# Optimization experiments

Hardware: AMD Instinct MI355X
Metric: run time of the kernel (lower is better)

## Reference

```python
import jax, jax.numpy as jnp
import numpy as np

GROUPS = 32
EPS = 1e-5

def setup_inputs() -> dict:
    key = jax.random.key(0)
    ks = jax.random.split(key, 10)
    B, H, W, C = 2, 64, 64, 512
    s = 1.0 / np.sqrt(C)
    return {
        "x": jax.random.normal(ks[0], (B, H, W, C), dtype=jnp.float32),
        "gamma": jnp.ones((C,), jnp.float32),
        "beta": jnp.zeros((C,), jnp.float32),
        "wq": jax.random.normal(ks[1], (C, C), jnp.float32) * s,
        "bq": jnp.zeros((C,), jnp.float32),
        "wk": jax.random.normal(ks[2], (C, C), jnp.float32) * s,
        "bk": jnp.zeros((C,), jnp.float32),
        "wv": jax.random.normal(ks[3], (C, C), jnp.float32) * s,
        "bv": jnp.zeros((C,), jnp.float32),
        "wp": jax.random.normal(ks[4], (C, C), jnp.float32) * s,
        "bp": jnp.zeros((C,), jnp.float32),
    }

def _group_norm(x, gamma, beta):
    B, H, W, C = x.shape
    xg = x.reshape(B, H, W, GROUPS, C // GROUPS)
    mean = jnp.mean(xg, axis=(1, 2, 4), keepdims=True)
    var = jnp.var(xg, axis=(1, 2, 4), keepdims=True)
    xg = (xg - mean) * jax.lax.rsqrt(var + EPS)
    return xg.reshape(B, H, W, C) * gamma + beta

def reference(x, gamma, beta, wq, bq, wk, bk, wv, bv, wp, bp):
    B, H, W, C = x.shape
    h_ = _group_norm(x, gamma, beta)
    # 1x1 convs are per-pixel linear maps
    q = jnp.einsum("bhwc,cd->bhwd", h_, wq) + bq
    k = jnp.einsum("bhwc,cd->bhwd", h_, wk) + bk
    v = jnp.einsum("bhwc,cd->bhwd", h_, wv) + bv
    q = q.reshape(B, H * W, C)
    k = k.reshape(B, H * W, C)
    v = v.reshape(B, H * W, C)
    scale = C ** (-0.5)
    attn = jax.nn.softmax(jnp.einsum("bqc,bkc->bqk", q, k) * scale, axis=-1)
    out = jnp.einsum("bqk,bkc->bqc", attn, v).reshape(B, H, W, C)
    proj = jnp.einsum("bhwc,cd->bhwd", out, wp) + bp
    return x + proj
```

## Files before the change

kernel.cpp:

```cpp
#include <hip/hip_runtime.h>
#include <hip/hip_bf16.h>
#include <cstdint>
#include <cstddef>

typedef __bf16 bf16;
typedef bf16 bf16x8 __attribute__((ext_vector_type(8)));
typedef bf16 bf16x4 __attribute__((ext_vector_type(4)));
typedef float floatx4 __attribute__((ext_vector_type(4)));
typedef int intx8 __attribute__((ext_vector_type(8)));
typedef int intx4 __attribute__((ext_vector_type(4)));

#define DEVI __device__ __forceinline__

#define C_  512
#define HW_ 4096
#define B_  2
#define M_  8192
#define TK  64


DEVI floatx4 mfma16(bf16x8 a, bf16x8 b, floatx4 c) {
  return __builtin_amdgcn_mfma_f32_16x16x32_bf16(a, b, c, 0, 0, 0);
}

DEVI floatx4 mfma_fp8(intx8 a, intx8 b, floatx4 c) {
  return __builtin_amdgcn_mfma_scale_f32_16x16x128_f8f6f4(a, b, c, 0, 0,
                                                          0, 127, 0, 127);
}

DEVI void gload16(const void* g, void* lds) {
  using gp = const __attribute__((address_space(1))) unsigned int*;
  using lp = __attribute__((address_space(3))) unsigned int*;
  __builtin_amdgcn_global_load_lds(
      reinterpret_cast<gp>(reinterpret_cast<uintptr_t>(g)),
      reinterpret_cast<lp>((unsigned int)(uintptr_t)lds), 16, 0, 0);
}

template <int N> DEVI void wait_vmcnt() {
  if constexpr (N == 0)       asm volatile("s_waitcnt vmcnt(0)" ::: "memory");
  else if constexpr (N == 6)  asm volatile("s_waitcnt vmcnt(6)" ::: "memory");
  else if constexpr (N == 8)  asm volatile("s_waitcnt vmcnt(8)" ::: "memory");
  else static_assert(N == 0, "unsupported vmcnt literal");
}

DEVI uint32_t f32_to_fp8(float x) {
  return (uint32_t)__builtin_amdgcn_cvt_pk_fp8_f32(x, x, 0, false) & 0xffu;
}
DEVI int pack4_fp8(float a, float b, float c, float d) {
  int pk = __builtin_amdgcn_cvt_pk_fp8_f32(a, b, 0, false);
  return __builtin_amdgcn_cvt_pk_fp8_f32(c, d, pk, true);
}

__global__ __launch_bounds__(256) void gn_part(const float* __restrict__ x,
                                               float* __restrict__ pp,
                                               float* __restrict__ l) {
  int blk = blockIdx.x;
  int t = threadIdx.x;
  if (t < 16) l[blk * 16 + t] = 0.f;
  int batch = blk >> 8;
  int pix0 = (blk & 255) * 16;
  int c4 = (t & 127) << 2;
  int ph = t >> 7;
  const float* px = x + (size_t)batch * HW_ * C_ + (size_t)(pix0 + ph) * C_ + c4;
  float s1 = 0.f, s2 = 0.f;
#pragma unroll
  for (int i = 0; i < 8; i++) {
    float4 v = *reinterpret_cast<const float4*>(px + (size_t)i * 2 * C_);
    s1 += v.x + v.y + v.z + v.w;
    s2 += v.x * v.x + v.y * v.y + v.z * v.z + v.w * v.w;
  }
  __shared__ float l1[256], l2[256];
  l1[t] = s1; l2[t] = s2;
  __syncthreads();
  if (t < 32) {
    float a = 0.f, b2 = 0.f;
#pragma unroll
    for (int j = 0; j < 4; j++) {
      a  += l1[t * 4 + j] + l1[t * 4 + j + 128];
      b2 += l2[t * 4 + j] + l2[t * 4 + j + 128];
    }
    pp[blk * 32 + t] = a;
    pp[512 * 32 + blk * 32 + t] = b2;
  }
}

__global__ __launch_bounds__(256) void finish_wtrans(
    const float* __restrict__ pp, float* __restrict__ stats,
    const float* __restrict__ wq, const float* __restrict__ wk,
    const float* __restrict__ wv, const float* __restrict__ wp,
    uint8_t* __restrict__ w8, bf16* __restrict__ wtp) {
  int t = threadIdx.x;
  if (blockIdx.x < 64) {
    int bg = blockIdx.x;
    int b = bg >> 5, g = bg & 31;
    float s1 = pp[(b * 256 + t) * 32 + g];
    float s2 = pp[512 * 32 + (b * 256 + t) * 32 + g];
    for (int off = 32; off; off >>= 1) {
      s1 += __shfl_down(s1, off);
      s2 += __shfl_down(s2, off);
    }
    __shared__ float r1[4], r2[4];
    int wid = t >> 6;
    if ((t & 63) == 0) { r1[wid] = s1; r2[wid] = s2; }
    __syncthreads();
    if (t == 0) {
      s1 = r1[0] + r1[1] + r1[2] + r1[3];
      s2 = r2[0] + r2[1] + r2[2] + r2[3];
      float inv = 1.0f / (HW_ * 16);
      float mean = s1 * inv;
      float var  = s2 * inv - mean * mean;
      stats[bg]      = mean;
      stats[64 + bg] = rsqrtf(var + 1e-5f);
    }
    return;
  }
  int id = blockIdx.x - 64;
  int z = id >> 8;
  int k0 = ((id >> 4) & 15) * 32, n0 = (id & 15) * 32;
  const float* w = (z == 0) ? wq : (z == 1) ? wk : (z == 2) ? wv : wp;
  __shared__ float tt[32][33];
  int r = t >> 5, cc = t & 31;
  for (int i = 0; i < 4; i++) {
    int rr = r + i * 8;
    tt[rr][cc] = w[(size_t)(k0 + rr) * C_ + n0 + cc];
  }
  __syncthreads();
  if (z < 3) {
    uint8_t* dst = w8 + (size_t)z * C_ * C_;
    for (int i = 0; i < 4; i++) {
      int rr = r + i * 8;
      dst[(size_t)(n0 + rr) * C_ + k0 + cc] = (uint8_t)f32_to_fp8(tt[cc][rr]);
    }
  } else {
    for (int i = 0; i < 4; i++) {
      int rr = r + i * 8;
      wtp[(size_t)(n0 + rr) * C_ + k0 + cc] = (bf16)tt[cc][rr];
    }
  }
}

__global__ __launch_bounds__(256) void gn_apply(const float* __restrict__ x,
                                                const float* __restrict__ gamma,
                                                const float* __restrict__ beta,
                                                const float* __restrict__ stats,
                                                uint8_t* __restrict__ h8) {
  int idx = blockIdx.x * 256 + threadIdx.x;
  int m  = idx >> 7;
  int c4 = (idx & 127) << 2;
  int b = m >> 12;
  int g = c4 >> 4;
  float mean = stats[(b << 5) + g];
  float rs   = stats[64 + (b << 5) + g];
  const float4 xv = *reinterpret_cast<const float4*>(x + (size_t)m * C_ + c4);
  const float4 gv = *reinterpret_cast<const float4*>(gamma + c4);
  const float4 bv = *reinterpret_cast<const float4*>(beta + c4);
  int pk = pack4_fp8((xv.x - mean) * rs * gv.x + bv.x,
                     (xv.y - mean) * rs * gv.y + bv.y,
                     (xv.z - mean) * rs * gv.z + bv.z,
                     (xv.w - mean) * rs * gv.w + bv.w);
  *reinterpret_cast<int*>(h8 + (size_t)m * C_ + c4) = pk;
}

template <int BM, int BN, int MT, int NT>
DEVI void gemm_main(const bf16* __restrict__ A, int lda,
                    const bf16* __restrict__ Bt, int ldb,
                    int K, floatx4 (&acc)[MT][NT]) {
  constexpr int WCOLS = BN / (NT * 16);
  constexpr int NLD = BM / 32 + BN / 32;
  static_assert(NLD == 6 || NLD == 8, "vmcnt literal supports 6/8");
  __shared__ __align__(16) bf16 As[2][BM * TK];
  __shared__ __align__(16) bf16 Bs[2][BN * TK];
  int tid = threadIdx.x;
  int w = tid >> 6, lane = tid & 63;
  int wrow = w / WCOLS, wcol = w % WCOLS;
  int col = lane & 15, quad = lane >> 4;
#pragma unroll
  for (int mt = 0; mt < MT; mt++)
#pragma unroll
    for (int nt = 0; nt < NT; nt++)
      acc[mt][nt] = floatx4{0.f, 0.f, 0.f, 0.f};

  auto stage = [&](int k0, bf16* as, bf16* bs) {
#pragma unroll
    for (int i = 0; i < BM / 32; i++) {
      int id = tid + i * 256;
      int r = id >> 3, wd = id & 7;
      gload16(A + (size_t)r * lda + k0 + ((wd ^ (r & 7)) << 3), as + id * 8);
    }
#pragma unroll
    for (int i = 0; i < BN / 32; i++) {
      int id = tid + i * 256;
      int r = id >> 3, wd = id & 7;
      gload16(Bt + (size_t)r * ldb + k0 + ((wd ^ (r & 7)) << 3), bs + id * 8);
    }
  };
  auto compute = [&](const bf16* sa, const bf16* sb) {
#pragma unroll
    for (int kk = 0; kk < 2; kk++) {
      bf16x8 af[MT], bfr[NT];
#pragma unroll
      for (int mt = 0; mt < MT; mt++) {
        int rA = wrow * MT * 16 + mt * 16 + col;
        af[mt] = *reinterpret_cast<const bf16x8*>(
            sa + rA * TK + (((kk * 4 + quad) ^ (rA & 7)) << 3));
      }
#pragma unroll
      for (int nt = 0; nt < NT; nt++) {
        int rB = wcol * NT * 16 + nt * 16 + col;
        bfr[nt] = *reinterpret_cast<const bf16x8*>(
            sb + rB * TK + (((kk * 4 + quad) ^ (rB & 7)) << 3));
      }
#pragma unroll
      for (int mt = 0; mt < MT; mt++)
#pragma unroll
        for (int nt = 0; nt < NT; nt++)
          acc[mt][nt] = mfma16(af[mt], bfr[nt], acc[mt][nt]);
    }
  };

  bf16 *s0a = &As[0][0], *s0b = &Bs[0][0];
  bf16 *s1a = &As[1][0], *s1b = &Bs[1][0];
  stage(0, s0a, s0b);
  int nIter = K / TK;
  for (int t = 0; t < nIter - 1; t++) {
    stage((t + 1) * TK, s1a, s1b);
    wait_vmcnt<NLD>();
    asm volatile("s_barrier" ::: "memory");
    compute(s0a, s0b);
    asm volatile("s_waitcnt lgkmcnt(0)" ::: "memory");
    asm volatile("s_barrier" ::: "memory");
    bf16* tp;
    tp = s0a; s0a = s1a; s1a = tp;
    tp = s0b; s0b = s1b; s1b = tp;
  }
  wait_vmcnt<0>();
  asm volatile("s_barrier" ::: "memory");
  compute(s0a, s0b);
}

template <int BM, int BN, int MT, int NT, int THREADS>
DEVI void gemm_fp8(const uint8_t* __restrict__ A, int lda,
                   const uint8_t* __restrict__ Bt, int ldb,
                   int K, floatx4 (&acc)[MT][NT]) {
  constexpr int WCOLS = BN / (NT * 16);
  constexpr int RPP = THREADS / 8;
  constexpr int NLD = (BM + BN) / RPP;
  static_assert(NLD == 6 || NLD == 8, "vmcnt literal supports 6/8");
  static_assert(BM % RPP == 0 && BN % RPP == 0, "stage pass mismatch");
  __shared__ __align__(16) uint8_t As[2][BM * 128];
  __shared__ __align__(16) uint8_t Bs[2][BN * 128];
  int tid = threadIdx.x;
  int w = tid >> 6, lane = tid & 63;
  int wrow = w / WCOLS, wcol = w % WCOLS;
  int col = lane & 15, quad = lane >> 4;
#pragma unroll
  for (int mt = 0; mt < MT; mt++)
#pragma unroll
    for (int nt = 0; nt < NT; nt++)
      acc[mt][nt] = floatx4{0.f, 0.f, 0.f, 0.f};

  auto stage = [&](int k0, uint8_t* as, uint8_t* bs) {
#pragma unroll
    for (int i = 0; i < BM / RPP; i++) {
      int id = tid + i * THREADS;
      int r = id >> 3, wd = id & 7;
      gload16(A + (size_t)r * lda + k0 + ((wd ^ (r & 7)) << 4), as + id * 16);
    }
#pragma unroll
    for (int i = 0; i < BN / RPP; i++) {
      int id = tid + i * THREADS;
      int r = id >> 3, wd = id & 7;
      gload16(Bt + (size_t)r * ldb + k0 + ((wd ^ (r & 7)) << 4), bs + id * 16);
    }
  };
  auto compute = [&](const uint8_t* sa, const uint8_t* sb) {
    intx8 af[MT], bfr[NT];
#pragma unroll
    for (int mt = 0; mt < MT; mt++) {
      int rA = wrow * MT * 16 + mt * 16 + col;
      const uint8_t* rowp = sa + (size_t)rA * 128;
      intx4 lo = *reinterpret_cast<const intx4*>(
          rowp + (((2 * quad) ^ (rA & 7)) << 4));
      intx4 hi = *reinterpret_cast<const intx4*>(
          rowp + (((2 * quad + 1) ^ (rA & 7)) << 4));
      af[mt] = __builtin_shufflevector(lo, hi, 0, 1, 2, 3, 4, 5, 6, 7);
    }
#pragma unroll
    for (int nt = 0; nt < NT; nt++) {
      int rB = wcol * NT * 16 + nt * 16 + col;
      const uint8_t* rowp = sb + (size_t)rB * 128;
      intx4 lo = *reinterpret_cast<const intx4*>(
          rowp + (((2 * quad) ^ (rB & 7)) << 4));
      intx4 hi = *reinterpret_cast<const intx4*>(
          rowp + (((2 * quad + 1) ^ (rB & 7)) << 4));
      bfr[nt] = __builtin_shufflevector(lo, hi, 0, 1, 2, 3, 4, 5, 6, 7);
    }
#pragma unroll
    for (int mt = 0; mt < MT; mt++)
#pragma unroll
      for (int nt = 0; nt < NT; nt++)
        acc[mt][nt] = mfma_fp8(af[mt], bfr[nt], acc[mt][nt]);
  };

  uint8_t *s0a = &As[0][0], *s0b = &Bs[0][0];
  uint8_t *s1a = &As[1][0], *s1b = &Bs[1][0];
  stage(0, s0a, s0b);
  int nIter = K >> 7;
  for (int t = 0; t < nIter - 1; t++) {
    stage((t + 1) << 7, s1a, s1b);
    wait_vmcnt<NLD>();
    asm volatile("s_barrier" ::: "memory");
    compute(s0a, s0b);
    asm volatile("s_waitcnt lgkmcnt(0)" ::: "memory");
    asm volatile("s_barrier" ::: "memory");
    uint8_t* tp;
    tp = s0a; s0a = s1a; s1a = tp;
    tp = s0b; s0b = s1b; s1b = tp;
  }
  wait_vmcnt<0>();
  asm volatile("s_barrier" ::: "memory");
  compute(s0a, s0b);
}

__global__ __launch_bounds__(256) void gemm_qkv(const uint8_t* __restrict__ h8,
                                                const uint8_t* __restrict__ w8,
                                                const float* __restrict__ bq,
                                                const float* __restrict__ bk,
                                                const float* __restrict__ bv,
                                                uint8_t* __restrict__ q8,
                                                uint8_t* __restrict__ k8,
                                                uint8_t* __restrict__ vt8) {
  int z = blockIdx.z;
  int m0 = blockIdx.x * 128, n0 = blockIdx.y * 128;
  floatx4 acc[4][4];
  gemm_fp8<128, 128, 4, 4, 256>(h8 + (size_t)m0 * C_, C_,
                                w8 + (size_t)z * C_ * C_ + (size_t)n0 * C_, C_,
                                C_, acc);
  int tid = threadIdx.x, w = tid >> 6, lane = tid & 63;
  int wrow = w >> 1, wcol = w & 1;
  int col = lane & 15, quad = lane >> 4;
  const float* bias = (z == 0) ? bq : (z == 1) ? bk : bv;
  if (z < 2) {
    uint8_t* out = (z == 0) ? q8 : k8;
#pragma unroll
    for (int mt = 0; mt < 4; mt++)
#pragma unroll
      for (int nt = 0; nt < 4; nt++) {
        int n = n0 + wcol * 64 + nt * 16 + col;
        float bb = bias[n];
#pragma unroll
        for (int r = 0; r < 4; r++) {
          int m = m0 + wrow * 64 + mt * 16 + quad * 4 + r;
          out[(size_t)m * C_ + n] = (uint8_t)f32_to_fp8(acc[mt][nt][r] + bb);
        }
      }
  } else {
#pragma unroll
    for (int mt = 0; mt < 4; mt++)
#pragma unroll
      for (int nt = 0; nt < 4; nt++) {
        int n = n0 + wcol * 64 + nt * 16 + col;
        float bb = bias[n];
        int mbase = m0 + wrow * 64 + mt * 16 + quad * 4;
        int b = mbase >> 12;
        int s = mbase & 4095;
        int pk = pack4_fp8(acc[mt][nt][0] + bb, acc[mt][nt][1] + bb,
                           acc[mt][nt][2] + bb, acc[mt][nt][3] + bb);
        *reinterpret_cast<int*>(vt8 + ((size_t)b * C_ + n) * HW_ + s) = pk;
      }
  }
}

__global__ __launch_bounds__(512) void gemm_qk(const uint8_t* __restrict__ q8,
                                               const uint8_t* __restrict__ k8,
                                               uint8_t* __restrict__ P8,
                                               float* __restrict__ l) {
  int b = blockIdx.z;
  int fid = blockIdx.y * 16 + blockIdx.x;
  int nid = (fid & 7) * 64 + (fid >> 3);
  int m0 = (nid & 15) * 256, n0 = (nid >> 4) * 128;
  floatx4 acc[4][4];
  gemm_fp8<256, 128, 4, 4, 512>(q8 + ((size_t)b * HW_ + m0) * C_, C_,
                                k8 + ((size_t)b * HW_ + n0) * C_, C_, C_, acc);
  __shared__ __align__(16) uint8_t P_lds[256 * 128];
  int tid = threadIdx.x, w = tid >> 6, lane = tid & 63;
  int wrow = w >> 1, wcol = w & 1;
  int col = lane & 15, quad = lane >> 4;
  const float sl2e = 0.044194173824159216f * 1.4426950408889634f;
  uint8_t* Pb = P8 + (size_t)b * HW_ * HW_;
  float* lb = l + (size_t)b * HW_;
#pragma unroll
  for (int mt = 0; mt < 4; mt++) {
    float rs[4] = {0.f, 0.f, 0.f, 0.f};
    int mloc = wrow * 64 + mt * 16 + quad * 4;
#pragma unroll
    for (int nt = 0; nt < 4; nt++) {
      int nl = wcol * 64 + nt * 16 + col;
      float p0 = exp2f(acc[mt][nt][0] * sl2e);
      float p1 = exp2f(acc[mt][nt][1] * sl2e);
      float p2 = exp2f(acc[mt][nt][2] * sl2e);
      float p3 = exp2f(acc[mt][nt][3] * sl2e);
      int pk = pack4_fp8(p0, p1, p2, p3);
#pragma unroll
      for (int r = 0; r < 4; r++) {
        int mr = mloc + r;
        P_lds[mr * 128 + (((nl >> 4) ^ (mr & 7)) << 4) + (nl & 15)] =
            (uint8_t)((unsigned)pk >> (8 * r));
      }
      rs[0] += p0; rs[1] += p1; rs[2] += p2; rs[3] += p3;
    }
#pragma unroll
    for (int off = 1; off < 16; off <<= 1)
#pragma unroll
      for (int r = 0; r < 4; r++)
        rs[r] += __shfl_xor(rs[r], off);
    if (col == 0)
#pragma unroll
      for (int r = 0; r < 4; r++)
        atomicAdd(&lb[mloc + m0 + r], rs[r]);
  }
  __syncthreads();
#pragma unroll
  for (int i = 0; i < 4; i++) {
    int id = tid + i * 512;
    int row = id >> 3, seg = id & 7;
    intx4 v = *reinterpret_cast<const intx4*>(
        P_lds + row * 128 + ((seg ^ (row & 7)) << 4));
    *reinterpret_cast<intx4*>(Pb + (size_t)(m0 + row) * HW_ + n0 + seg * 16) = v;
  }
}

__global__ __launch_bounds__(256) void gemm_pv(const uint8_t* __restrict__ P8,
                                               const uint8_t* __restrict__ vt8,
                                               const float* __restrict__ l,
                                               bf16* __restrict__ o) {
  int b = blockIdx.z;
  int fid = blockIdx.y * 32 + blockIdx.x;
  int xcd = fid & 7, i = fid >> 3;
  int m0 = (xcd * 4 + (i & 3)) * 128;
  int n0 = (i >> 2) * 64;
  floatx4 acc[2][4];
  gemm_fp8<128, 64, 2, 4, 256>(P8 + (size_t)b * HW_ * HW_ + (size_t)m0 * HW_,
                               HW_, vt8 + ((size_t)b * C_ + n0) * HW_, HW_,
                               HW_, acc);
  int tid = threadIdx.x, w = tid >> 6, lane = tid & 63;
  int col = lane & 15, quad = lane >> 4;
  const float* lb = l + (size_t)b * HW_;
  bf16* ob = o + (size_t)b * HW_ * C_;
#pragma unroll
  for (int mt = 0; mt < 2; mt++)
#pragma unroll
    for (int r = 0; r < 4; r++) {
      int m = m0 + w * 32 + mt * 16 + quad * 4 + r;
      float inv = 1.0f / lb[m];
#pragma unroll
      for (int nt = 0; nt < 4; nt++) {
        int n = n0 + nt * 16 + col;
        ob[(size_t)m * C_ + n] = (bf16)(acc[mt][nt][r] * inv);
      }
    }
}

__global__ __launch_bounds__(256) void gemm_proj(const bf16* __restrict__ o,
                                                 const bf16* __restrict__ wtp,
                                                 const float* __restrict__ bp,
                                                 const float* __restrict__ x,
                                                 float* __restrict__ out) {
  int m0 = blockIdx.x * 128, n0 = blockIdx.y * 64;
  floatx4 acc[2][4];
  gemm_main<128, 64, 2, 4>(o + (size_t)m0 * C_, C_, wtp + (size_t)n0 * C_, C_, C_, acc);
  int tid = threadIdx.x, w = tid >> 6, lane = tid & 63;
  int col = lane & 15, quad = lane >> 4;
#pragma unroll
  for (int mt = 0; mt < 2; mt++)
#pragma unroll
    for (int nt = 0; nt < 4; nt++) {
      int n = n0 + nt * 16 + col;
      float bb = bp[n];
#pragma unroll
      for (int r = 0; r < 4; r++) {
        int m = m0 + w * 32 + mt * 16 + quad * 4 + r;
        out[(size_t)m * C_ + n] = x[(size_t)m * C_ + n] + acc[mt][nt][r] + bb;
      }
    }
}

extern "C" void kernel_launch(void* const* d_in, const int* in_sizes, int n_in,
                              void* d_out, int out_size, void* d_ws, size_t ws_size,
                              hipStream_t stream) {
  const float* x     = (const float*)d_in[0];
  const float* gamma = (const float*)d_in[1];
  const float* beta  = (const float*)d_in[2];
  const float* wq    = (const float*)d_in[3];
  const float* bq    = (const float*)d_in[4];
  const float* wk    = (const float*)d_in[5];
  const float* bk    = (const float*)d_in[6];
  const float* wv    = (const float*)d_in[7];
  const float* bv    = (const float*)d_in[8];
  const float* wp    = (const float*)d_in[9];
  const float* bp    = (const float*)d_in[10];
  float* out = (float*)d_out;

  char* w8s = (char*)d_ws;
  float* stats = (float*)(w8s);
  float* l     = (float*)(w8s + 65536u);
  float* pp    = (float*)(w8s + 393216u);
  uint8_t* w8  = (uint8_t*)(w8s + (1u << 20));
  bf16* wtp    = (bf16*)(w8s + (2u << 20));
  uint8_t* h8  = (uint8_t*)(w8s + (4u << 20));
  bf16* o      = (bf16*)(w8s + (8u << 20));
  uint8_t* q8  = (uint8_t*)(w8s + (16u << 20));
  uint8_t* k8  = (uint8_t*)(w8s + (20u << 20));
  uint8_t* vt8 = (uint8_t*)(w8s + (24u << 20));
  uint8_t* P8  = (uint8_t*)(w8s + (28u << 20));

  gn_part<<<512, 256, 0, stream>>>(x, pp, l);
  finish_wtrans<<<1088, 256, 0, stream>>>(pp, stats, wq, wk, wv, wp, w8, wtp);
  gn_apply<<<4096, 256, 0, stream>>>(x, gamma, beta, stats, h8);
  gemm_qkv<<<dim3(M_ / 128, C_ / 128, 3), 256, 0, stream>>>(h8, w8, bq, bk, bv, q8, k8, vt8);
  gemm_qk<<<dim3(HW_ / 256, HW_ / 128, B_), 512, 0, stream>>>(q8, k8, P8, l);
  gemm_pv<<<dim3(HW_ / 128, C_ / 64, B_), 256, 0, stream>>>(P8, vt8, l, o);
  gemm_proj<<<dim3(M_ / 128, C_ / 64, 1), 256, 0, stream>>>(o, wtp, bp, x, out);
}
```

Before: 178.5 us.

## Fuse QK softmax and PV into a single flash-style attention kernel

Replaces the separate QK^T kernel, which wrote a full fp8 probability matrix to global memory along with atomically accumulated row sums, and the PV kernel that read it back. The new kernel has each block own 32 query rows. It loops over key tiles, computes scores with fp8 MFMA, exponentiates into LDS, and accumulates P·V in registers, then normalizes by row sums reduced in LDS. This removes the 32MB P round trip, the atomics and a launch. In exchange there are only 256 blocks, K/V are loaded straight from global with no LDS staging or prefetch, and each key tile needs two barriers. No max subtraction is done, as before.

```diff
diff --git a/kernel.cpp b/kernel.cpp
--- a/kernel.cpp
+++ b/kernel.cpp
@@ -5,7 +5,6 @@
 
 typedef __bf16 bf16;
 typedef bf16 bf16x8 __attribute__((ext_vector_type(8)));
-typedef bf16 bf16x4 __attribute__((ext_vector_type(4)));
 typedef float floatx4 __attribute__((ext_vector_type(4)));
 typedef int intx8 __attribute__((ext_vector_type(8)));
 typedef int intx4 __attribute__((ext_vector_type(4)));
@@ -52,11 +51,9 @@
 }
 
 __global__ __launch_bounds__(256) void gn_part(const float* __restrict__ x,
-                                               float* __restrict__ pp,
-                                               float* __restrict__ l) {
+                                               float* __restrict__ pp) {
   int blk = blockIdx.x;
   int t = threadIdx.x;
-  if (t < 16) l[blk * 16 + t] = 0.f;
   int batch = blk >> 8;
   int pix0 = (blk & 255) * 16;
   int c4 = (t & 127) << 2;
@@ -371,92 +368,152 @@
   }
 }
 
-__global__ __launch_bounds__(512) void gemm_qk(const uint8_t* __restrict__ q8,
-                                               const uint8_t* __restrict__ k8,
-                                               uint8_t* __restrict__ P8,
-                                               float* __restrict__ l) {
+__global__ __launch_bounds__(512) void attn_fused(const uint8_t* __restrict__ q8,
+                                                  const uint8_t* __restrict__ k8,
+                                                  const uint8_t* __restrict__ vt8,
+                                                  bf16* __restrict__ o) {
   int b = blockIdx.z;
-  int fid = blockIdx.y * 16 + blockIdx.x;
-  int nid = (fid & 7) * 64 + (fid >> 3);
-  int m0 = (nid & 15) * 256, n0 = (nid >> 4) * 128;
-  floatx4 acc[4][4];
-  gemm_fp8<256, 128, 4, 4, 512>(q8 + ((size_t)b * HW_ + m0) * C_, C_,
-                                k8 + ((size_t)b * HW_ + n0) * C_, C_, C_, acc);
-  __shared__ __align__(16) uint8_t P_lds[256 * 128];
-  int tid = threadIdx.x, w = tid >> 6, lane = tid & 63;
-  int wrow = w >> 1, wcol = w & 1;
+  int m0 = blockIdx.x * 32;
+  __shared__ __align__(16) uint8_t Qs[32 * 512];
+  __shared__ __align__(16) uint8_t P_lds[32 * 128];
+  __shared__ float l_lds[8][32];
+  int tid = threadIdx.x;
+  int w = tid >> 6, lane = tid & 63;
   int col = lane & 15, quad = lane >> 4;
+
+  const uint8_t* qb = q8 + ((size_t)b * HW_ + m0) * C_;
+#pragma unroll
+  for (int i = 0; i < 2; i++) {
+    int id = tid + i * 512;
+    int r = id >> 5, wd = id & 31;
+    gload16(qb + (size_t)r * C_ + ((wd ^ (r & 7)) << 4), Qs + id * 16);
+  }
+
+  floatx4 O[2][4];
+#pragma unroll
+  for (int mt = 0; mt < 2; mt++)
+#pragma unroll
+    for (int cf = 0; cf < 4; cf++)
+      O[mt][cf] = floatx4{0.f, 0.f, 0.f, 0.f};
+  float lp[2][4] = {{0.f, 0.f, 0.f, 0.f}, {0.f, 0.f, 0.f, 0.f}};
+
   const float sl2e = 0.044194173824159216f * 1.4426950408889634f;
-  uint8_t* Pb = P8 + (size_t)b * HW_ * HW_;
-  float* lb = l + (size_t)b * HW_;
-#pragma unroll
-  for (int mt = 0; mt < 4; mt++) {
-    float rs[4] = {0.f, 0.f, 0.f, 0.f};
-    int mloc = wrow * 64 + mt * 16 + quad * 4;
-#pragma unroll
-    for (int nt = 0; nt < 4; nt++) {
-      int nl = wcol * 64 + nt * 16 + col;
-      float p0 = exp2f(acc[mt][nt][0] * sl2e);
-      float p1 = exp2f(acc[mt][nt][1] * sl2e);
-      float p2 = exp2f(acc[mt][nt][2] * sl2e);
-      float p3 = exp2f(acc[mt][nt][3] * sl2e);
+  const uint8_t* kb = k8 + (size_t)b * HW_ * C_;
+  const uint8_t* vb = vt8 + (size_t)b * C_ * HW_;
+
+  wait_vmcnt<0>();
+  asm volatile("s_barrier" ::: "memory");
+
+  for (int kt = 0; kt < 32; kt++) {
+    int s0 = kt * 128;
+    intx8 kf[4];
+#pragma unroll
+    for (int ks = 0; ks < 4; ks++) {
+      const uint8_t* krow =
+          kb + (size_t)(s0 + w * 16 + col) * C_ + ks * 128 + quad * 32;
+      intx4 lo = *reinterpret_cast<const intx4*>(krow);
+      intx4 hi = *reinterpret_cast<const intx4*>(krow + 16);
+      kf[ks] = __builtin_shufflevector(lo, hi, 0, 1, 2, 3, 4, 5, 6, 7);
+    }
+    floatx4 sacc[2];
+    sacc[0] = floatx4{0.f, 0.f, 0.f, 0.f};
+    sacc[1] = floatx4{0.f, 0.f, 0.f, 0.f};
+#pragma unroll
+    for (int mt = 0; mt < 2; mt++) {
+      int m = mt * 16 + col;
+      const uint8_t* qrow = Qs + (size_t)m * 512;
+      int mm = m & 7;
+#pragma unroll
+      for (int ks = 0; ks < 4; ks++) {
+        intx4 lo = *reinterpret_cast<const intx4*>(
+            qrow + ((ks * 8 + ((2 * quad) ^ mm)) << 4));
+        intx4 hi = *reinterpret_cast<const intx4*>(
+            qrow + ((ks * 8 + ((2 * quad + 1) ^ mm)) << 4));
+        intx8 af = __builtin_shufflevector(lo, hi, 0, 1, 2, 3, 4, 5, 6, 7);
+        sacc[mt] = mfma_fp8(af, kf[ks], sacc[mt]);
+      }
+    }
+    intx8 vf[4];
+#pragma unroll
+    for (int cf = 0; cf < 4; cf++) {
+      const uint8_t* vrow =
+          vb + (size_t)(w * 64 + cf * 16 + col) * HW_ + s0 + quad * 32;
+      intx4 lo = *reinterpret_cast<const intx4*>(vrow);
+      intx4 hi = *reinterpret_cast<const intx4*>(vrow + 16);
+      vf[cf] = __builtin_shufflevector(lo, hi, 0, 1, 2, 3, 4, 5, 6, 7);
+    }
+#pragma unroll
+    for (int mt = 0; mt < 2; mt++) {
+      float p0 = exp2f(sacc[mt][0] * sl2e);
+      float p1 = exp2f(sacc[mt][1] * sl2e);
+      float p2 = exp2f(sacc[mt][2] * sl2e);
+      float p3 = exp2f(sacc[mt][3] * sl2e);
       int pk = pack4_fp8(p0, p1, p2, p3);
 #pragma unroll
       for (int r = 0; r < 4; r++) {
-        int mr = mloc + r;
-        P_lds[mr * 128 + (((nl >> 4) ^ (mr & 7)) << 4) + (nl & 15)] =
+        int m = mt * 16 + quad * 4 + r;
+        P_lds[m * 128 + (((w) ^ (m & 7)) << 4) + col] =
             (uint8_t)((unsigned)pk >> (8 * r));
       }
-      rs[0] += p0; rs[1] += p1; rs[2] += p2; rs[3] += p3;
-    }
-#pragma unroll
-    for (int off = 1; off < 16; off <<= 1)
+      lp[mt][0] += p0; lp[mt][1] += p1; lp[mt][2] += p2; lp[mt][3] += p3;
+    }
+    asm volatile("s_waitcnt lgkmcnt(0)" ::: "memory");
+    asm volatile("s_barrier" ::: "memory");
+    intx8 paf[2];
+#pragma unroll
+    for (int mt = 0; mt < 2; mt++) {
+      int m = mt * 16 + col;
+      int mm = m & 7;
+      intx4 lo = *reinterpret_cast<const intx4*>(
+          P_lds + m * 128 + (((2 * quad) ^ mm) << 4));
+      intx4 hi = *reinterpret_cast<const intx4*>(
+          P_lds + m * 128 + (((2 * quad + 1) ^ mm) << 4));
+      paf[mt] = __builtin_shufflevector(lo, hi, 0, 1, 2, 3, 4, 5, 6, 7);
+    }
+#pragma unroll
+    for (int mt = 0; mt < 2; mt++)
+#pragma unroll
+      for (int cf = 0; cf < 4; cf++)
+        O[mt][cf] = mfma_fp8(paf[mt], vf[cf], O[mt][cf]);
+    asm volatile("s_waitcnt lgkmcnt(0)" ::: "memory");
+    asm volatile("s_barrier" ::: "memory");
+  }
+#pragma unroll
+  for (int mt = 0; mt < 2; mt++)
+#pragma unroll
+    for (int r = 0; r < 4; r++)
+#pragma unroll
+      for (int off = 1; off < 16; off <<= 1)
+        lp[mt][r] += __shfl_xor(lp[mt][r], off);
+  if (col == 0) {
+#pragma unroll
+    for (int mt = 0; mt < 2; mt++)
 #pragma unroll
       for (int r = 0; r < 4; r++)
-        rs[r] += __shfl_xor(rs[r], off);
-    if (col == 0)
-#pragma unroll
-      for (int r = 0; r < 4; r++)
-        atomicAdd(&lb[mloc + m0 + r], rs[r]);
+        l_lds[w][mt * 16 + quad * 4 + r] = lp[mt][r];
   }
   __syncthreads();
-#pragma unroll
-  for (int i = 0; i < 4; i++) {
-    int id = tid + i * 512;
-    int row = id >> 3, seg = id & 7;
-    intx4 v = *reinterpret_cast<const intx4*>(
-        P_lds + row * 128 + ((seg ^ (row & 7)) << 4));
-    *reinterpret_cast<intx4*>(Pb + (size_t)(m0 + row) * HW_ + n0 + seg * 16) = v;
-  }
-}
-
-__global__ __launch_bounds__(256) void gemm_pv(const uint8_t* __restrict__ P8,
-                                               const uint8_t* __restrict__ vt8,
-                                               const float* __restrict__ l,
-                                               bf16* __restrict__ o) {
-  int b = blockIdx.z;
-  int fid = blockIdx.y * 32 + blockIdx.x;
-  int xcd = fid & 7, i = fid >> 3;
-  int m0 = (xcd * 4 + (i & 3)) * 128;
-  int n0 = (i >> 2) * 64;
-  floatx4 acc[2][4];
-  gemm_fp8<128, 64, 2, 4, 256>(P8 + (size_t)b * HW_ * HW_ + (size_t)m0 * HW_,
-                               HW_, vt8 + ((size_t)b * C_ + n0) * HW_, HW_,
-                               HW_, acc);
-  int tid = threadIdx.x, w = tid >> 6, lane = tid & 63;
-  int col = lane & 15, quad = lane >> 4;
-  const float* lb = l + (size_t)b * HW_;
-  bf16* ob = o + (size_t)b * HW_ * C_;
+  float inv[2][4];
 #pragma unroll
   for (int mt = 0; mt < 2; mt++)
 #pragma unroll
     for (int r = 0; r < 4; r++) {
-      int m = m0 + w * 32 + mt * 16 + quad * 4 + r;
-      float inv = 1.0f / lb[m];
-#pragma unroll
-      for (int nt = 0; nt < 4; nt++) {
-        int n = n0 + nt * 16 + col;
-        ob[(size_t)m * C_ + n] = (bf16)(acc[mt][nt][r] * inv);
+      int m = mt * 16 + quad * 4 + r;
+      float s = 0.f;
+#pragma unroll
+      for (int ww = 0; ww < 8; ww++) s += l_lds[ww][m];
+      inv[mt][r] = 1.0f / s;
+    }
+  bf16* ob = o + ((size_t)b * HW_ + m0) * C_;
+#pragma unroll
+  for (int mt = 0; mt < 2; mt++)
+#pragma unroll
+    for (int cf = 0; cf < 4; cf++) {
+      int c = w * 64 + cf * 16 + col;
+#pragma unroll
+      for (int r = 0; r < 4; r++) {
+        int m = mt * 16 + quad * 4 + r;
+        ob[(size_t)m * C_ + c] = (bf16)(O[mt][cf][r] * inv[mt][r]);
       }
     }
 }
@@ -503,7 +560,6 @@
 
   char* w8s = (char*)d_ws;
   float* stats = (float*)(w8s);
-  float* l     = (float*)(w8s + 65536u);
   float* pp    = (float*)(w8s + 393216u);
   uint8_t* w8  = (uint8_t*)(w8s + (1u << 20));
   bf16* wtp    = (bf16*)(w8s + (2u << 20));
@@ -512,13 +568,11 @@
   uint8_t* q8  = (uint8_t*)(w8s + (16u << 20));
   uint8_t* k8  = (uint8_t*)(w8s + (20u << 20));
   uint8_t* vt8 = (uint8_t*)(w8s + (24u << 20));
-  uint8_t* P8  = (uint8_t*)(w8s + (28u << 20));
-
-  gn_part<<<512, 256, 0, stream>>>(x, pp, l);
+
+  gn_part<<<512, 256, 0, stream>>>(x, pp);
   finish_wtrans<<<1088, 256, 0, stream>>>(pp, stats, wq, wk, wv, wp, w8, wtp);
   gn_apply<<<4096, 256, 0, stream>>>(x, gamma, beta, stats, h8);
   gemm_qkv<<<dim3(M_ / 128, C_ / 128, 3), 256, 0, stream>>>(h8, w8, bq, bk, bv, q8, k8, vt8);
-  gemm_qk<<<dim3(HW_ / 256, HW_ / 128, B_), 512, 0, stream>>>(q8, k8, P8, l);
-  gemm_pv<<<dim3(HW_ / 128, C_ / 64, B_), 256, 0, stream>>>(P8, vt8, l, o);
+  attn_fused<<<dim3(HW_ / 32, 1, B_), 512, 0, stream>>>(q8, k8, vt8, o);
   gemm_proj<<<dim3(M_ / 128, C_ / 64, 1), 256, 0, stream>>>(o, wtp, bp, x, out);
 }
```

Result: slower. 235.2 us (+31.8%).
